# Kernel tuning notes

Measured on AMD Instinct MI355X. Metric: run time of the kernel, lower is better.

Reference implementation:

```python
import jax, jax.numpy as jnp
import numpy as np

N_CLASS = 81          # 80 foreground classes + background (class 0)
R = 1000              # test-time RoIs from RPN
IMG_H, IMG_W = 600.0, 800.0   # original_size
SCORE_THRESH = 0.05
NMS_THRESH = 0.5
LOC_STD = jnp.array([0.1, 0.1, 0.2, 0.2], dtype=jnp.float32)
LOC_MEAN = jnp.zeros(4, dtype=jnp.float32)


def setup_inputs() -> dict:
    key = jax.random.key(0)
    k1, k2, k3, k4 = jax.random.split(key, 4)
    # rois in (ymin, xmin, ymax, xmax) within the image
    yx = jax.random.uniform(k1, (R, 2), dtype=jnp.float32) * jnp.array([IMG_H * 0.8, IMG_W * 0.8])
    hw = jax.random.uniform(k2, (R, 2), dtype=jnp.float32) * jnp.array([IMG_H * 0.2, IMG_W * 0.2]) + 1.0
    roi = jnp.concatenate([yx, yx + hw], axis=1)                       # [R, 4]
    roi_loc = jax.random.normal(k3, (R, N_CLASS * 4), dtype=jnp.float32)
    roi_score = jax.random.normal(k4, (R, N_CLASS), dtype=jnp.float32) * 2.0
    return {"roi": roi, "roi_loc": roi_loc, "roi_score": roi_score}


def _loc2bbox(roi, loc):
    # roi [R,4] (ymin,xmin,ymax,xmax); loc [R,C,4] (dy,dx,dh,dw) -> bbox [R,C,4]
    h = roi[:, 2] - roi[:, 0]
    w = roi[:, 3] - roi[:, 1]
    cy = roi[:, 0] + 0.5 * h
    cx = roi[:, 1] + 0.5 * w
    dy, dx, dh, dw = loc[..., 0], loc[..., 1], loc[..., 2], loc[..., 3]
    ctr_y = dy * h[:, None] + cy[:, None]
    ctr_x = dx * w[:, None] + cx[:, None]
    nh = jnp.exp(dh) * h[:, None]
    nw = jnp.exp(dw) * w[:, None]
    return jnp.stack([ctr_y - 0.5 * nh, ctr_x - 0.5 * nw,
                      ctr_y + 0.5 * nh, ctr_x + 0.5 * nw], axis=-1)


def _nms_per_class(boxes, scores):
    # boxes [R,4], scores [R] -> (sorted boxes, sorted scores, keep mask)
    order = jnp.argsort(-scores)
    b = boxes[order]
    s = scores[order]
    valid = s > SCORE_THRESH
    area = (b[:, 2] - b[:, 0]) * (b[:, 3] - b[:, 1])
    tl = jnp.maximum(b[:, None, :2], b[None, :, :2])
    br = jnp.minimum(b[:, None, 2:], b[None, :, 2:])
    wh = jnp.clip(br - tl, 0.0)
    inter = wh[..., 0] * wh[..., 1]
    iou = inter / (area[:, None] + area[None, :] - inter + 1e-9)   # [R,R]
    idx = jnp.arange(R)

    def body(i, keep):
        sup = keep[i] & (iou[i] > NMS_THRESH) & (idx > i)
        return keep & ~sup

    keep = jax.lax.fori_loop(0, R, body, valid)
    return b, s, keep


def reference(roi, roi_loc, roi_score):
    loc = roi_loc.reshape(R, N_CLASS, 4) * LOC_STD + LOC_MEAN
    bbox = _loc2bbox(roi, loc)                                   # [R, C, 4]
    # clamp: even coords (y) to [0, H], odd coords (x) to [0, W]
    hi = jnp.array([IMG_H, IMG_W, IMG_H, IMG_W], dtype=bbox.dtype)
    bbox = jnp.clip(bbox, 0.0, hi)
    prob = jax.nn.softmax(roi_score, axis=1)                     # [R, C]
    # per-class suppression, skipping background class 0
    boxes_c = jnp.swapaxes(bbox, 0, 1)[1:]                       # [C-1, R, 4]
    scores_c = prob.T[1:]                                        # [C-1, R]
    b, s, keep = jax.vmap(_nms_per_class)(boxes_c, scores_c)
    out = jnp.where(keep[..., None],
                    jnp.concatenate([b, s[..., None]], axis=-1), 0.0)  # [C-1, R, 5]
    labels = jnp.broadcast_to(jnp.arange(N_CLASS - 1, dtype=jnp.int32)[:, None], keep.shape)
    labels = jnp.where(keep, labels, -1)
    return out, labels
```

## Files before the change

kernel.cpp:

```cpp
#include <hip/hip_runtime.h>
#include <math.h>

#define R 1000
#define NC 81
#define MAXP 1024
#define NT 256
#define SUPMAX 512
#define WMAX 8

__global__ __launch_bounds__(256) void softmax_stats_kernel(
    const float* __restrict__ roi_score,
    float* __restrict__ wsmax,
    float* __restrict__ wsrcp)
{
    const int wid  = threadIdx.x >> 6;
    const int lane = threadIdx.x & 63;
    const int r    = blockIdx.x * 4 + wid;
    if (r >= R) return;
    const float* sc = roi_score + r * NC;
    float v0 = sc[lane];
    float v1 = (lane < NC - 64) ? sc[lane + 64] : -INFINITY;
    float m = fmaxf(v0, v1);
    #pragma unroll
    for (int off = 32; off > 0; off >>= 1)
        m = fmaxf(m, __shfl_xor(m, off, 64));
    float e = expf(v0 - m) + ((lane < NC - 64) ? expf(v1 - m) : 0.0f);
    #pragma unroll
    for (int off = 32; off > 0; off >>= 1)
        e += __shfl_xor(e, off, 64);
    if (lane == 0) {
        wsmax[r] = m;
        wsrcp[r] = 1.0f / e;
    }
}

__global__ __launch_bounds__(NT) void frcnn_class_kernel(
    const float* __restrict__ roi,
    const float* __restrict__ roi_loc,
    const float* __restrict__ roi_score,
    const float* __restrict__ wsmax,
    const float* __restrict__ wsrcp,
    float* __restrict__ out)
{
    const int c   = blockIdx.x + 1;
    const int tid = threadIdx.x;

    __shared__ float s_score[MAXP];
    __shared__ int   s_idx[MAXP];
    __shared__ float s_y0[MAXP], s_x0[MAXP], s_y1[MAXP], s_x1[MAXP], s_area[MAXP];
    __shared__ int   s_keepi[MAXP];
    __shared__ unsigned long long s_sup[SUPMAX * WMAX];
    __shared__ unsigned long long s_kw[WMAX];
    __shared__ int   s_cnt;

    if (tid == 0) s_cnt = 0;
    __syncthreads();

    for (int r = tid; r < R; r += NT) {
        float p = expf(roi_score[r * NC + c] - wsmax[r]) * wsrcp[r];
        if (p > 0.05f) {
            int slot = atomicAdd(&s_cnt, 1);
            s_score[slot] = p;
            s_idx[slot]   = r;
        }
    }
    __syncthreads();
    const int V = s_cnt;

    int P = 2;
    while (P < V) P <<= 1;
    for (int t = V + tid; t < P; t += NT) {
        s_score[t] = -INFINITY;
        s_idx[t]   = R + t;
    }
    __syncthreads();

    for (int k = 2; k <= P; k <<= 1) {
        for (int j = k >> 1; j > 0; j >>= 1) {
            for (int i = tid; i < P; i += NT) {
                int ixj = i ^ j;
                if (ixj > i) {
                    float si = s_score[i], sx = s_score[ixj];
                    int   ii = s_idx[i],   ix = s_idx[ixj];
                    bool after_i = (sx > si) || (sx == si && ix < ii);
                    bool doswap  = ((i & k) == 0) ? after_i : !after_i;
                    if (doswap) {
                        s_score[i] = sx; s_score[ixj] = si;
                        s_idx[i]   = ix; s_idx[ixj]   = ii;
                    }
                }
            }
            __syncthreads();
        }
    }

    for (int p = tid; p < V; p += NT) {
        int r = s_idx[p];
        float ry0 = roi[r*4+0], rx0 = roi[r*4+1];
        float ry1 = roi[r*4+2], rx1 = roi[r*4+3];
        float h = ry1 - ry0, w = rx1 - rx0;
        float cy = ry0 + 0.5f*h, cx = rx0 + 0.5f*w;
        const float* lp = roi_loc + (size_t)r*(NC*4) + c*4;
        float dy = lp[0]*0.1f, dx = lp[1]*0.1f;
        float dh = lp[2]*0.2f, dw = lp[3]*0.2f;
        float ny = dy*h + cy, nx = dx*w + cx;
        float nh = expf(dh)*h, nw = expf(dw)*w;
        float y0 = ny - 0.5f*nh, x0 = nx - 0.5f*nw;
        float y1 = ny + 0.5f*nh, x1 = nx + 0.5f*nw;
        y0 = fminf(fmaxf(y0, 0.f), 600.f);
        x0 = fminf(fmaxf(x0, 0.f), 800.f);
        y1 = fminf(fmaxf(y1, 0.f), 600.f);
        x1 = fminf(fmaxf(x1, 0.f), 800.f);
        s_y0[p] = y0; s_x0[p] = x0; s_y1[p] = y1; s_x1[p] = x1;
        s_area[p] = (y1 - y0) * (x1 - x0);
        s_keepi[p] = 1;
    }
    __syncthreads();

    if (V > 0 && V <= SUPMAX) {
        const int W = (V + 63) >> 6;
        for (int u = tid; u < V * W; u += NT) {
            int i = u / W;
            int w = u - i * W;
            int j0 = w * 64;
            int js = (i + 1 > j0) ? i + 1 : j0;
            int je = (j0 + 64 < V) ? j0 + 64 : V;
            unsigned long long bits = 0ull;
            float ay0 = s_y0[i], ax0 = s_x0[i];
            float ay1 = s_y1[i], ax1 = s_x1[i];
            float aa  = s_area[i];
            for (int j = js; j < je; ++j) {
                float ty = fmaxf(ay0, s_y0[j]);
                float tx = fmaxf(ax0, s_x0[j]);
                float by = fminf(ay1, s_y1[j]);
                float bx = fminf(ax1, s_x1[j]);
                float hh = fmaxf(by - ty, 0.f);
                float ww = fmaxf(bx - tx, 0.f);
                float inter = hh * ww;
                float iou = inter / (aa + s_area[j] - inter + 1e-9f);
                if (iou > 0.5f) bits |= (1ull << (j - j0));
            }
            s_sup[i * W + w] = bits;
        }
        if (tid < W) {
            int full = V - tid * 64;
            s_kw[tid] = (full >= 64) ? ~0ull : ((1ull << full) - 1ull);
        }
        __syncthreads();
        if (tid == 0) {
            int curw = 0;
            unsigned long long cur = s_kw[0];
            for (int i = 0; i < V; ++i) {
                int w = i >> 6;
                if (w != curw) { s_kw[curw] = cur; cur = s_kw[w]; curw = w; }
                if ((cur >> (i & 63)) & 1ull) {
                    #pragma unroll
                    for (int ww = 0; ww < WMAX; ++ww) {
                        if (ww < W) {
                            unsigned long long msk = ~s_sup[i * W + ww];
                            if (ww == curw) cur &= msk;
                            else           s_kw[ww] &= msk;
                        }
                    }
                }
            }
            s_kw[curw] = cur;
        }
        __syncthreads();
        for (int p = tid; p < V; p += NT)
            s_keepi[p] = (int)((s_kw[p >> 6] >> (p & 63)) & 1ull);
        __syncthreads();
    } else if (V > SUPMAX) {
        for (int i = 0; i < V; ++i) {
            if (s_keepi[i]) {
                float ay0 = s_y0[i], ax0 = s_x0[i];
                float ay1 = s_y1[i], ax1 = s_x1[i];
                float aa  = s_area[i];
                for (int jj = i + 1 + tid; jj < V; jj += NT) {
                    float ty = fmaxf(ay0, s_y0[jj]);
                    float tx = fmaxf(ax0, s_x0[jj]);
                    float by = fminf(ay1, s_y1[jj]);
                    float bx = fminf(ax1, s_x1[jj]);
                    float hh = fmaxf(by - ty, 0.f);
                    float ww = fmaxf(bx - tx, 0.f);
                    float inter = hh * ww;
                    float iou = inter / (aa + s_area[jj] - inter + 1e-9f);
                    if (iou > 0.5f) s_keepi[jj] = 0;
                }
            }
            __syncthreads();
        }
    }

    float* out0 = out + (size_t)(c - 1) * R * 5;
    float* out1 = out + (size_t)80 * R * 5 + (size_t)(c - 1) * R;
    for (int p = tid; p < R; p += NT) {
        float y0 = 0.f, x0 = 0.f, y1 = 0.f, x1 = 0.f, s = 0.f, lab = -1.0f;
        if (p < V && s_keepi[p]) {
            y0 = s_y0[p]; x0 = s_x0[p]; y1 = s_y1[p]; x1 = s_x1[p];
            s  = s_score[p];
            lab = (float)(c - 1);
        }
        out0[p*5+0] = y0; out0[p*5+1] = x0; out0[p*5+2] = y1;
        out0[p*5+3] = x1; out0[p*5+4] = s;
        out1[p] = lab;
    }
}

extern "C" void kernel_launch(void* const* d_in, const int* in_sizes, int n_in,
                              void* d_out, int out_size, void* d_ws, size_t ws_size,
                              hipStream_t stream) {
    const float* roi       = (const float*)d_in[0];
    const float* roi_loc   = (const float*)d_in[1];
    const float* roi_score = (const float*)d_in[2];
    float* out   = (float*)d_out;
    float* wsmax = (float*)d_ws;
    float* wsrcp = wsmax + 1024;

    hipLaunchKernelGGL(softmax_stats_kernel, dim3((R + 3) / 4), dim3(256), 0, stream,
                       roi_score, wsmax, wsrcp);
    hipLaunchKernelGGL(frcnn_class_kernel, dim3(NC - 1), dim3(NT), 0, stream,
                       roi, roi_loc, roi_score, wsmax, wsrcp, out);
}
```

Before: 94.98 us.

## Replace bitonic sort with rank-based scatter and restructure NMS mask build

Replaces the multi-pass bitonic sort, which needed many barriers, with an O(V^2) rank computation: each thread counts how many candidates beat its own and scatters its decoded box into that sorted slot. The block size grows to 512 threads. The suppression-mask build now gives each thread one row instead of one (row, word) pair. The serial greedy sweep keeps the keep-words in registers and only updates later words. The rank loop does quadratic shared-memory reads per thread in exchange for removing the sort barriers, and the serial sweep is still single-threaded.

Result: faster. 87.68 us (-7.7%).

```diff
diff --git a/kernel.cpp b/kernel.cpp
--- a/kernel.cpp
+++ b/kernel.cpp
@@ -4,7 +4,7 @@
 #define R 1000
 #define NC 81
 #define MAXP 1024
-#define NT 256
+#define NT 512
 #define SUPMAX 512
 #define WMAX 8
 
@@ -47,6 +47,7 @@
 
     __shared__ float s_score[MAXP];
     __shared__ int   s_idx[MAXP];
+    __shared__ float s_ss[MAXP];
     __shared__ float s_y0[MAXP], s_x0[MAXP], s_y1[MAXP], s_x1[MAXP], s_area[MAXP];
     __shared__ int   s_keepi[MAXP];
     __shared__ unsigned long long s_sup[SUPMAX * WMAX];
@@ -67,40 +68,20 @@
     __syncthreads();
     const int V = s_cnt;
 
-    int P = 2;
-    while (P < V) P <<= 1;
-    for (int t = V + tid; t < P; t += NT) {
-        s_score[t] = -INFINITY;
-        s_idx[t]   = R + t;
-    }
-    __syncthreads();
-
-    for (int k = 2; k <= P; k <<= 1) {
-        for (int j = k >> 1; j > 0; j >>= 1) {
-            for (int i = tid; i < P; i += NT) {
-                int ixj = i ^ j;
-                if (ixj > i) {
-                    float si = s_score[i], sx = s_score[ixj];
-                    int   ii = s_idx[i],   ix = s_idx[ixj];
-                    bool after_i = (sx > si) || (sx == si && ix < ii);
-                    bool doswap  = ((i & k) == 0) ? after_i : !after_i;
-                    if (doswap) {
-                        s_score[i] = sx; s_score[ixj] = si;
-                        s_idx[i]   = ix; s_idx[ixj]   = ii;
-                    }
-                }
-            }
-            __syncthreads();
-        }
-    }
-
     for (int p = tid; p < V; p += NT) {
-        int r = s_idx[p];
-        float ry0 = roi[r*4+0], rx0 = roi[r*4+1];
-        float ry1 = roi[r*4+2], rx1 = roi[r*4+3];
+        float sp = s_score[p];
+        int   ip = s_idx[p];
+        int rank = 0;
+        for (int q = 0; q < V; ++q) {
+            float sq = s_score[q];
+            int   iq = s_idx[q];
+            rank += (sq > sp) || (sq == sp && iq < ip);
+        }
+        float ry0 = roi[ip*4+0], rx0 = roi[ip*4+1];
+        float ry1 = roi[ip*4+2], rx1 = roi[ip*4+3];
         float h = ry1 - ry0, w = rx1 - rx0;
         float cy = ry0 + 0.5f*h, cx = rx0 + 0.5f*w;
-        const float* lp = roi_loc + (size_t)r*(NC*4) + c*4;
+        const float* lp = roi_loc + (size_t)ip*(NC*4) + c*4;
         float dy = lp[0]*0.1f, dx = lp[1]*0.1f;
         float dh = lp[2]*0.2f, dw = lp[3]*0.2f;
         float ny = dy*h + cy, nx = dx*w + cx;
@@ -111,64 +92,67 @@
         x0 = fminf(fmaxf(x0, 0.f), 800.f);
         y1 = fminf(fmaxf(y1, 0.f), 600.f);
         x1 = fminf(fmaxf(x1, 0.f), 800.f);
-        s_y0[p] = y0; s_x0[p] = x0; s_y1[p] = y1; s_x1[p] = x1;
-        s_area[p] = (y1 - y0) * (x1 - x0);
-        s_keepi[p] = 1;
+        s_ss[rank] = sp;
+        s_y0[rank] = y0; s_x0[rank] = x0; s_y1[rank] = y1; s_x1[rank] = x1;
+        s_area[rank] = (y1 - y0) * (x1 - x0);
+        s_keepi[rank] = 1;
     }
     __syncthreads();
 
     if (V > 0 && V <= SUPMAX) {
         const int W = (V + 63) >> 6;
-        for (int u = tid; u < V * W; u += NT) {
-            int i = u / W;
-            int w = u - i * W;
-            int j0 = w * 64;
-            int js = (i + 1 > j0) ? i + 1 : j0;
-            int je = (j0 + 64 < V) ? j0 + 64 : V;
-            unsigned long long bits = 0ull;
+        for (int i = tid; i < V; i += NT) {
             float ay0 = s_y0[i], ax0 = s_x0[i];
             float ay1 = s_y1[i], ax1 = s_x1[i];
             float aa  = s_area[i];
-            for (int j = js; j < je; ++j) {
-                float ty = fmaxf(ay0, s_y0[j]);
-                float tx = fmaxf(ax0, s_x0[j]);
-                float by = fminf(ay1, s_y1[j]);
-                float bx = fminf(ax1, s_x1[j]);
-                float hh = fmaxf(by - ty, 0.f);
-                float ww = fmaxf(bx - tx, 0.f);
-                float inter = hh * ww;
-                float iou = inter / (aa + s_area[j] - inter + 1e-9f);
-                if (iou > 0.5f) bits |= (1ull << (j - j0));
-            }
-            s_sup[i * W + w] = bits;
-        }
-        if (tid < W) {
-            int full = V - tid * 64;
-            s_kw[tid] = (full >= 64) ? ~0ull : ((1ull << full) - 1ull);
+            for (int w = 0; w < W; ++w) {
+                int j0 = w * 64;
+                int js = (i + 1 > j0) ? i + 1 : j0;
+                int je = (j0 + 64 < V) ? j0 + 64 : V;
+                unsigned long long bits = 0ull;
+                for (int j = js; j < je; ++j) {
+                    float ty = fmaxf(ay0, s_y0[j]);
+                    float tx = fmaxf(ax0, s_x0[j]);
+                    float by = fminf(ay1, s_y1[j]);
+                    float bx = fminf(ax1, s_x1[j]);
+                    float hh = fmaxf(by - ty, 0.f);
+                    float ww = fmaxf(bx - tx, 0.f);
+                    float inter = hh * ww;
+                    float iou = inter / (aa + s_area[j] - inter + 1e-9f);
+                    if (iou > 0.5f) bits |= (1ull << (j - j0));
+                }
+                s_sup[i * W + w] = bits;
+            }
         }
         __syncthreads();
         if (tid == 0) {
-            int curw = 0;
-            unsigned long long cur = s_kw[0];
-            for (int i = 0; i < V; ++i) {
-                int w = i >> 6;
-                if (w != curw) { s_kw[curw] = cur; cur = s_kw[w]; curw = w; }
-                if ((cur >> (i & 63)) & 1ull) {
-                    #pragma unroll
-                    for (int ww = 0; ww < WMAX; ++ww) {
-                        if (ww < W) {
-                            unsigned long long msk = ~s_sup[i * W + ww];
-                            if (ww == curw) cur &= msk;
-                            else           s_kw[ww] &= msk;
+            unsigned long long kw[WMAX];
+            #pragma unroll
+            for (int w = 0; w < WMAX; ++w) {
+                int full = V - w * 64;
+                kw[w] = (full >= 64) ? ~0ull : (full > 0 ? ((1ull << full) - 1ull) : 0ull);
+            }
+            #pragma unroll
+            for (int w = 0; w < WMAX; ++w) {
+                if (w * 64 < V) {
+                    unsigned long long cur = kw[w];
+                    int lim = V - w * 64; if (lim > 64) lim = 64;
+                    for (int b = 0; b < lim; ++b) {
+                        if ((cur >> b) & 1ull) {
+                            const unsigned long long* row = &s_sup[(w * 64 + b) * W];
+                            cur &= ~row[w];
+                            #pragma unroll
+                            for (int w2 = 0; w2 < WMAX; ++w2) {
+                                if (w2 > w) { if (w2 < W) kw[w2] &= ~row[w2]; }
+                            }
                         }
                     }
+                    kw[w] = cur;
                 }
             }
-            s_kw[curw] = cur;
-        }
-        __syncthreads();
-        for (int p = tid; p < V; p += NT)
-            s_keepi[p] = (int)((s_kw[p >> 6] >> (p & 63)) & 1ull);
+            #pragma unroll
+            for (int w = 0; w < WMAX; ++w) s_kw[w] = kw[w];
+        }
         __syncthreads();
     } else if (V > SUPMAX) {
         for (int i = 0; i < V; ++i) {
@@ -192,13 +176,18 @@
         }
     }
 
+    const bool matrix_path = (V <= SUPMAX);
     float* out0 = out + (size_t)(c - 1) * R * 5;
     float* out1 = out + (size_t)80 * R * 5 + (size_t)(c - 1) * R;
     for (int p = tid; p < R; p += NT) {
+        bool kept = false;
+        if (p < V)
+            kept = matrix_path ? (((s_kw[p >> 6] >> (p & 63)) & 1ull) != 0ull)
+                               : (s_keepi[p] != 0);
         float y0 = 0.f, x0 = 0.f, y1 = 0.f, x1 = 0.f, s = 0.f, lab = -1.0f;
-        if (p < V && s_keepi[p]) {
+        if (kept) {
             y0 = s_y0[p]; x0 = s_x0[p]; y1 = s_y1[p]; x1 = s_x1[p];
-            s  = s_score[p];
+            s  = s_ss[p];
             lab = (float)(c - 1);
         }
         out0[p*5+0] = y0; out0[p*5+1] = x0; out0[p*5+2] = y1;
```
